# Optimization experiments

Hardware: AMD Instinct MI355X
Metric: run time of the kernel (lower is better)

The kernel has to match this reference:

```python
import jax, jax.numpy as jnp
import numpy as np

C0 = 1.0  # speed of sound (units absorbed; distances pre-scaled)
FS = 1.0  # sampling frequency

A, E, S = 4, 128, 3072   # n_angles, n_elements, n_samples
NZ, NX = 512, 256        # image grid


def setup_inputs() -> dict:
    key = jax.random.key(0)
    k1, k2, k3, k4 = jax.random.split(key, 4)
    scale = (S / 2.0) - 1.0  # spread delays over the valid sample range
    d_tx = jax.random.uniform(k1, (A, NZ, NX), dtype=jnp.float32) * scale
    d_rx = jax.random.uniform(k2, (E, NZ, NX), dtype=jnp.float32) * scale
    apod = jax.random.uniform(k3, (E, NZ, NX), dtype=jnp.float32)
    rf = jax.random.normal(k4, (A, E, S), dtype=jnp.float32)
    t0 = jnp.zeros((A,), dtype=jnp.float32)
    return {"d_tx": d_tx, "d_rx": d_rx, "apod": apod, "rf": rf, "t0": t0}


def reference(d_tx, d_rx, apod, rf, t0):
    a, e, s = rf.shape
    nz, nx = d_tx.shape[1], d_tx.shape[2]
    # total delay in samples: [A, E, nz, nx]
    delays = ((d_tx[:, None] + d_rx[None]) / C0 - t0[:, None, None, None]) * FS
    x0 = jnp.floor(delays)
    w = delays - x0                      # linear interp weight
    i0 = x0.astype(jnp.int32)
    i1 = i0 + 1

    def gather(idx):
        # rf: [A, E, S]; idx: [A, E, nz, nx] -> gathered [A, E, nz, nx]
        g = jnp.take_along_axis(rf, jnp.clip(idx, 0, s - 1).reshape(a, e, -1), axis=2)
        return g.reshape(a, e, nz, nx)

    # grid_sample(padding_mode='zeros', align_corners=True): out-of-range taps contribute 0
    v0 = jnp.where((i0 >= 0) & (i0 <= s - 1), gather(i0), 0.0)
    v1 = jnp.where((i1 >= 0) & (i1 <= s - 1), gather(i1), 0.0)
    sampled = v0 * (1.0 - w) + v1 * w    # [A, E, nz, nx]
    # apodization-weighted sum over elements -> [A, nz, nx]
    das = jnp.einsum('aezx,ezx->azx', sampled, apod)
    return das
```

## Files before the change

kernel.cpp:

```cpp
#include <hip/hip_runtime.h>


#define A_N 4
#define E_N 128
#define S_N 3072
#define NPIX_N (512 * 256)
#define TPB 1024
#define PXT 4
#define TILE (TPB * PXT)
#define TILES (NPIX_N / TILE)
#define ESPLIT 8
#define EPB (E_N / ESPLIT)
#define CPA (S_N / 256)
#define CHUNKS (A_N * CPA)
#define WAVES (TPB / 64)
#define CPW (CHUNKS / WAVES)

__device__ __forceinline__ void ld_lds16(const float* g, float* l) {
    __builtin_amdgcn_global_load_lds(
        (const __attribute__((address_space(1))) void*)g,
        (__attribute__((address_space(3))) void*)l, 16, 0, 0);
}

__global__ __launch_bounds__(TPB) void das_kernel(
    const float* __restrict__ d_tx, const float* __restrict__ d_rx,
    const float* __restrict__ apod, const float* __restrict__ rf,
    const float* __restrict__ t0,  float* __restrict__ out)
{
    __shared__ float lds_rf[2][A_N * S_N];
    const int tid  = threadIdx.x;
    const int wid  = tid >> 6;
    const int lane = tid & 63;
    const int px0  = blockIdx.x * TILE + tid;
    const int e0   = blockIdx.y * EPB;

    auto stage = [&](int b, int e) {
#pragma unroll
        for (int j = 0; j < CPW; ++j) {
            const int chunk = wid * CPW + j;
            const int a = chunk / CPA;
            const int c = chunk - a * CPA;
            const float* g = rf + ((size_t)(a * E_N + e)) * S_N + c * 256 + lane * 4;
            float* l = &lds_rf[b][a * S_N + c * 256];
            ld_lds16(g, l);
        }
    };

    stage(0, e0);

    float acc[A_N][PXT];
    float dta[A_N][PXT];
#pragma unroll
    for (int a = 0; a < A_N; ++a) {
        const float t0a = t0[a];
#pragma unroll
        for (int k = 0; k < PXT; ++k) {
            dta[a][k] = d_tx[a * NPIX_N + px0 + k * TPB] - t0a;
            acc[a][k] = 0.0f;
        }
    }

    float ndrx[PXT], nap[PXT];
#pragma unroll
    for (int k = 0; k < PXT; ++k) {
        ndrx[k] = d_rx[(size_t)e0 * NPIX_N + px0 + k * TPB];
        nap[k]  = apod[(size_t)e0 * NPIX_N + px0 + k * TPB];
    }

    __syncthreads();

    for (int ei = 0; ei < EPB; ++ei) {
        const int e   = e0 + ei;
        const int cur = ei & 1;

        float drx[PXT], ap[PXT];
#pragma unroll
        for (int k = 0; k < PXT; ++k) { drx[k] = ndrx[k]; ap[k] = nap[k]; }

        if (ei + 1 < EPB) {
            stage(cur ^ 1, e + 1);
            const float* __restrict__ nd = d_rx + (size_t)(e + 1) * NPIX_N;
            const float* __restrict__ na = apod + (size_t)(e + 1) * NPIX_N;
#pragma unroll
            for (int k = 0; k < PXT; ++k) {
                ndrx[k] = nd[px0 + k * TPB];
                nap[k]  = na[px0 + k * TPB];
            }
        }

        const float* __restrict__ L = lds_rf[cur];
#pragma unroll
        for (int k = 0; k < PXT; ++k) {
#pragma unroll
            for (int a = 0; a < A_N; ++a) {
                float delay = dta[a][k] + drx[k];
                float x0 = floorf(delay);
                float w  = delay - x0;
                int i0 = (int)x0;
                i0 = min(max(i0, 0), S_N - 2);
                float v0 = L[a * S_N + i0];
                float v1 = L[a * S_N + i0 + 1];
                acc[a][k] += (v0 + w * (v1 - v0)) * ap[k];
            }
        }

        __syncthreads();
    }

#pragma unroll
    for (int a = 0; a < A_N; ++a)
#pragma unroll
        for (int k = 0; k < PXT; ++k)
            atomicAdd(&out[a * NPIX_N + px0 + k * TPB], acc[a][k]);
}

extern "C" void kernel_launch(void* const* d_in, const int* in_sizes, int n_in,
                              void* d_out, int out_size, void* d_ws, size_t ws_size,
                              hipStream_t stream) {
    const float* d_tx = (const float*)d_in[0];
    const float* d_rx = (const float*)d_in[1];
    const float* apod = (const float*)d_in[2];
    const float* rf   = (const float*)d_in[3];
    const float* t0   = (const float*)d_in[4];
    float* out = (float*)d_out;

    hipMemsetAsync(out, 0, (size_t)out_size * sizeof(float), stream);
    dim3 grid(TILES, ESPLIT);
    das_kernel<<<grid, TPB, 0, stream>>>(d_tx, d_rx, apod, rf, t0, out);
}
```

Before: 180.9 us.

## Store RF in LDS as fp16 sample pairs for single-load interpolation

Staging of RF into LDS changes from direct global-to-LDS copies to register loads that are converted into packed fp16 pairs (sample i, sample i+1). Each interpolation then needs one 32-bit LDS read instead of two float reads. The aim is to halve LDS gather traffic and instruction count, which likely dominate. In exchange, RF values lose precision in fp16, and staging now goes through registers with conversion work and register pressure, done after the compute phase.

```diff
diff --git a/kernel.cpp b/kernel.cpp
--- a/kernel.cpp
+++ b/kernel.cpp
@@ -11,42 +11,53 @@
 #define TILES (NPIX_N / TILE)
 #define ESPLIT 8
 #define EPB (E_N / ESPLIT)
-#define CPA (S_N / 256)
-#define CHUNKS (A_N * CPA)
-#define WAVES (TPB / 64)
-#define CPW (CHUNKS / WAVES)
+#define SIT ((A_N * (S_N / 4)) / TPB)
 
-__device__ __forceinline__ void ld_lds16(const float* g, float* l) {
-    __builtin_amdgcn_global_load_lds(
-        (const __attribute__((address_space(1))) void*)g,
-        (__attribute__((address_space(3))) void*)l, 16, 0, 0);
-}
+typedef __fp16 half2_t __attribute__((ext_vector_type(2)));
 
 __global__ __launch_bounds__(TPB) void das_kernel(
     const float* __restrict__ d_tx, const float* __restrict__ d_rx,
     const float* __restrict__ apod, const float* __restrict__ rf,
     const float* __restrict__ t0,  float* __restrict__ out)
 {
-    __shared__ float lds_rf[2][A_N * S_N];
-    const int tid  = threadIdx.x;
-    const int wid  = tid >> 6;
-    const int lane = tid & 63;
-    const int px0  = blockIdx.x * TILE + tid;
-    const int e0   = blockIdx.y * EPB;
+    __shared__ __align__(16) half2_t lds_rf[2][A_N * S_N];
+    const int tid = threadIdx.x;
+    const int px0 = blockIdx.x * TILE + tid;
+    const int e0  = blockIdx.y * EPB;
 
-    auto stage = [&](int b, int e) {
+    int s_a[SIT], s_s4[SIT];
 #pragma unroll
-        for (int j = 0; j < CPW; ++j) {
-            const int chunk = wid * CPW + j;
-            const int a = chunk / CPA;
-            const int c = chunk - a * CPA;
-            const float* g = rf + ((size_t)(a * E_N + e)) * S_N + c * 256 + lane * 4;
-            float* l = &lds_rf[b][a * S_N + c * 256];
-            ld_lds16(g, l);
+    for (int j = 0; j < SIT; ++j) {
+        int idx = tid + j * TPB;
+        s_a[j]  = idx / (S_N / 4);
+        s_s4[j] = idx - s_a[j] * (S_N / 4);
+    }
+
+    float4 pf[SIT];
+    float  pe[SIT];
+    auto load_rf = [&](int e) {
+#pragma unroll
+        for (int j = 0; j < SIT; ++j) {
+            const float* r = rf + ((size_t)(s_a[j] * E_N + e)) * S_N + s_s4[j] * 4;
+            pf[j] = *(const float4*)r;
+            pe[j] = r[(s_s4[j] == (S_N / 4 - 1)) ? 3 : 4];
+        }
+    };
+    auto write_rf = [&](int b) {
+#pragma unroll
+        for (int j = 0; j < SIT; ++j) {
+            float4 v = pf[j];
+            float  x = pe[j];
+            union { half2_t h[4]; float4 f; } u;
+            u.h[0] = half2_t{(__fp16)v.x, (__fp16)v.y};
+            u.h[1] = half2_t{(__fp16)v.y, (__fp16)v.z};
+            u.h[2] = half2_t{(__fp16)v.z, (__fp16)v.w};
+            u.h[3] = half2_t{(__fp16)v.w, (__fp16)x};
+            *(float4*)&lds_rf[b][s_a[j] * S_N + s_s4[j] * 4] = u.f;
         }
     };
 
-    stage(0, e0);
+    load_rf(e0);
 
     float acc[A_N][PXT];
     float dta[A_N][PXT];
@@ -67,6 +78,7 @@
         nap[k]  = apod[(size_t)e0 * NPIX_N + px0 + k * TPB];
     }
 
+    write_rf(0);
     __syncthreads();
 
     for (int ei = 0; ei < EPB; ++ei) {
@@ -78,7 +90,7 @@
         for (int k = 0; k < PXT; ++k) { drx[k] = ndrx[k]; ap[k] = nap[k]; }
 
         if (ei + 1 < EPB) {
-            stage(cur ^ 1, e + 1);
+            load_rf(e + 1);
             const float* __restrict__ nd = d_rx + (size_t)(e + 1) * NPIX_N;
             const float* __restrict__ na = apod + (size_t)(e + 1) * NPIX_N;
 #pragma unroll
@@ -88,7 +100,7 @@
             }
         }
 
-        const float* __restrict__ L = lds_rf[cur];
+        const half2_t* __restrict__ L = lds_rf[cur];
 #pragma unroll
         for (int k = 0; k < PXT; ++k) {
 #pragma unroll
@@ -98,11 +110,14 @@
                 float w  = delay - x0;
                 int i0 = (int)x0;
                 i0 = min(max(i0, 0), S_N - 2);
-                float v0 = L[a * S_N + i0];
-                float v1 = L[a * S_N + i0 + 1];
+                half2_t hv = L[a * S_N + i0];
+                float v0 = (float)hv[0];
+                float v1 = (float)hv[1];
                 acc[a][k] += (v0 + w * (v1 - v0)) * ap[k];
             }
         }
+
+        if (ei + 1 < EPB) write_rf(cur ^ 1);
 
         __syncthreads();
     }
```

After: 187.6 us. 3.7% more time.
